# Performance work log

Measured on AMD Instinct MI355X. Metric: run time of the kernel, lower is better.

Reference implementation:

```python
import jax, jax.numpy as jnp
import numpy as np
from functools import partial

B, C, H, W = 256, 3, 128, 128

def _conv(x, w, b, pad):
    y = jax.lax.conv_general_dilated(x, w, (1, 1), [(pad, pad), (pad, pad)],
                                     dimension_numbers=('NCHW', 'OIHW', 'NCHW'))
    return y + b[None, :, None, None]

def _maxpool2(x):
    return jax.lax.reduce_window(x, -jnp.inf, jax.lax.max, (1, 1, 2, 2), (1, 1, 2, 2), 'VALID')

def _linear(x, w, b):
    return x @ w.T + b

def _handcrafted(images):
    # uint8 quantization: floor(x*255); inputs in [0,1) so no wraparound
    img8 = jnp.floor(images * 255.0)                      # [B,3,H,W]
    brightness = img8.mean(axis=(-2, -1))                 # [B,3]
    contrast = img8.std(axis=(-2, -1))                    # [B,3] (ddof=0, numpy default)
    # cv2.Sobel ksize=3, BORDER_REFLECT_101 == jnp.pad 'reflect'; cv2 does correlation
    kx = jnp.array([[-1., 0., 1.], [-2., 0., 2.], [-1., 0., 1.]], dtype=img8.dtype)
    ky = kx.T
    k = jnp.stack([kx, ky])[:, None]                      # [2,1,3,3]
    p = jnp.pad(img8, ((0, 0), (0, 0), (1, 1), (1, 1)), mode='reflect')
    s = jax.lax.conv_general_dilated(p.reshape(B * 3, 1, H + 2, W + 2), k, (1, 1),
                                     'VALID', dimension_numbers=('NCHW', 'OIHW', 'NCHW'))
    edge = jnp.sqrt(s[:, 0] ** 2 + s[:, 1] ** 2).mean(axis=(-2, -1)).reshape(B, 3)
    return jnp.concatenate([edge, brightness, contrast], axis=1)  # [B,9]

def setup_inputs() -> dict:
    key = jax.random.key(0)
    ks = jax.random.split(key, 20)
    g = lambda i, shape, fan: (jax.random.normal(ks[i], shape, jnp.float32) * (1.0 / np.sqrt(fan)))
    return {
        'images': jax.random.uniform(ks[0], (B, C, H, W), jnp.float32),
        'W1': g(1, (32, 3, 3, 3), 27), 'b1': jnp.zeros((32,), jnp.float32),
        'W2': g(2, (64, 32, 3, 3), 288), 'b2': jnp.zeros((64,), jnp.float32),
        'Wa': g(3, (1, 64, 7, 7), 64 * 49), 'ba': jnp.zeros((1,), jnp.float32),
        'Wfc': g(4, (50, 64 * 32 * 32), 64 * 32 * 32), 'bfc': jnp.zeros((50,), jnp.float32),
        'Wh1': g(5, (32, 9), 9), 'bh1': jnp.zeros((32,), jnp.float32),
        'Wh2': g(6, (64, 32), 32), 'bh2': jnp.zeros((64,), jnp.float32),
        'Wh3': g(7, (50, 64), 64), 'bh3': jnp.zeros((50,), jnp.float32),
        'Wf': g(8, (64, 100), 100), 'bf': jnp.zeros((64,), jnp.float32),
        'Wc': g(9, (1, 64), 64), 'bc': jnp.zeros((1,), jnp.float32),
    }

def reference(images, W1, b1, W2, b2, Wa, ba, Wfc, bfc,
              Wh1, bh1, Wh2, bh2, Wh3, bh3, Wf, bf, Wc, bc):
    # CNN branch
    x = jax.nn.relu(_conv(images, W1, b1, 1))
    x = _maxpool2(x)
    x = jax.nn.relu(_conv(x, W2, b2, 1))
    x = _maxpool2(x)                                      # [B,64,32,32]
    attn = jax.nn.sigmoid(_conv(x, Wa, ba, 3))            # spatial attention
    x = x * attn
    cnn_feat = jax.nn.relu(_linear(x.reshape(B, -1), Wfc, bfc))  # [B,50]
    # handcrafted branch
    f = _handcrafted(images)                              # [B,9]
    h = jax.nn.relu(_linear(f, Wh1, bh1))
    h = jax.nn.relu(_linear(h, Wh2, bh2))
    h = jax.nn.relu(_linear(h, Wh3, bh3))                 # [B,50]
    fused = jax.nn.relu(_linear(jnp.concatenate([cnn_feat, h], axis=1), Wf, bf))
    logits = _linear(fused, Wc, bc)
    return jax.nn.sigmoid(logits)
```

## Files before the change

kernel.cpp:

```cpp
#include <hip/hip_runtime.h>
#include <stdint.h>

typedef __bf16 bf16x8 __attribute__((ext_vector_type(8)));
typedef float f32x4 __attribute__((ext_vector_type(4)));

__device__ inline float bf2f(uint16_t u) {
    uint32_t x = ((uint32_t)u) << 16;
    float f;
    __builtin_memcpy(&f, &x, 4);
    return f;
}
__device__ inline uint16_t f2bf(float f) {
    uint32_t x;
    __builtin_memcpy(&x, &f, 4);
    uint32_t r = (x + 0x7FFFu + ((x >> 16) & 1u)) >> 16;
    return (uint16_t)r;
}

__global__ __launch_bounds__(256) void k_prep_small(const float* __restrict__ W2,
                                                    const float* __restrict__ W1,
                                                    const float* __restrict__ Wa,
                                                    uint16_t* __restrict__ wA,
                                                    uint16_t* __restrict__ wA1c,
                                                    uint16_t* __restrict__ waP) {
    int bid = blockIdx.x;
    int tid = threadIdx.x;
    if (bid < 72) {
        int j = bid * 256 + tid;
        if (j >= 18432) return;
        int t = j >> 11, rem = j & 2047, oc = rem >> 5, ic = rem & 31;
        int dy = t / 3, dx = t - dy * 3;
        wA[j] = f2bf(W2[(oc * 32 + ic) * 9 + dy * 3 + dx]);
    } else if (bid < 84) {
        int j = (bid - 72) * 256 + tid;
        if (j >= 3072) return;
        int dy = j >> 10, rem = j & 1023, oc = rem >> 5, k = rem & 31;
        int dx = k >> 2, ic = k & 3;
        uint16_t v = 0;
        if (dx < 3 && ic < 3) v = f2bf(W1[((oc * 3 + ic) * 3 + dy) * 3 + dx]);
        wA1c[j] = v;
    } else {
        int j = (bid - 84) * 256 + tid;
        if (j >= 4096) return;
        int chunk = j >> 10, ks = (j >> 9) & 1, tl = (j >> 5) & 15, ch = j & 31;
        int t = chunk * 16 + tl;
        int cg = ks * 32 + ch;
        waP[j] = (t < 49) ? f2bf(Wa[cg * 49 + t]) : (uint16_t)0;
    }
}

__global__ __launch_bounds__(256) void k_prep_wfc(const float* __restrict__ Wfc,
                                                  uint16_t* __restrict__ wfcb) {
    int o = blockIdx.x;
    int pb = blockIdx.y;
    int ch = threadIdx.x & 63;
    int pr = threadIdx.x >> 6;
    const float* src = Wfc + (size_t)o * 65536 + ch * 1024;
    uint16_t* dst = wfcb + (size_t)o * 65536 + ch;
#pragma unroll 4
    for (int i = 0; i < 16; ++i) {
        int px = pb * 64 + i * 4 + pr;
        dst[(size_t)px * 64] = f2bf(src[px]);
    }
}

__global__ __launch_bounds__(256) void k_handcrafted(const float* __restrict__ img,
                                                     float* __restrict__ f) {
    __shared__ float p[128 * 129];
    int c = blockIdx.x, b = blockIdx.y;
    const float* src = img + (((size_t)(b * 3 + c)) << 14);
    int tid = threadIdx.x;
    float sum = 0.f, sumsq = 0.f;
    for (int it = 0; it < 64; ++it) {
        int idx = tid + (it << 8);
        int r = idx >> 7, cc = idx & 127;
        float v = floorf(src[idx] * 255.0f);
        p[r * 129 + cc] = v;
        sum += v;
        sumsq += v * v;
    }
    __syncthreads();
    {
        int r = tid >> 1;
        int c0 = (tid & 1) * 64;
        int rm = (r == 0) ? 1 : (r - 1), rp = (r == 127) ? 126 : (r + 1);
        const float* Pm = &p[rm * 129];
        const float* P0 = &p[r * 129];
        const float* Pp = &p[rp * 129];
        float am, a0, ap, bm, b0, bp, cm, c0v, cp;
        if (c0 == 0) {
            a0 = Pm[0]; ap = Pm[1]; am = ap;
            b0 = P0[0]; bp = P0[1]; bm = bp;
            c0v = Pp[0]; cp = Pp[1]; cm = cp;
        } else {
            am = Pm[63]; a0 = Pm[64]; ap = Pm[65];
            bm = P0[63]; b0 = P0[64]; bp = P0[65];
            cm = Pp[63]; c0v = Pp[64]; cp = Pp[65];
        }
        float esum = 0.f;
        for (int i = 0; i < 64; ++i) {
            float gx = (ap - am) + 2.f * (bp - bm) + (cp - cm);
            float gy = (cm + 2.f * c0v + cp) - (am + 2.f * a0 + ap);
            esum += sqrtf(gx * gx + gy * gy);
            if (i < 63) {
                int nc = c0 + i + 2;
                am = a0; a0 = ap;
                bm = b0; b0 = bp;
                cm = c0v; c0v = cp;
                if (nc <= 127) {
                    ap = Pm[nc];
                    bp = P0[nc];
                    cp = Pp[nc];
                } else {
                    ap = am;
                    bp = bm;
                    cp = cm;
                }
            }
        }
        for (int off = 32; off; off >>= 1) {
            sum += __shfl_down(sum, off);
            sumsq += __shfl_down(sumsq, off);
            esum += __shfl_down(esum, off);
        }
        __syncthreads();
        int w = tid >> 6;
        if ((tid & 63) == 0) {
            p[w * 3 + 0] = sum;
            p[w * 3 + 1] = sumsq;
            p[w * 3 + 2] = esum;
        }
        __syncthreads();
        if (tid == 0) {
            float S = 0.f, Q = 0.f, E = 0.f;
            for (int i = 0; i < 4; ++i) {
                S += p[i * 3 + 0];
                Q += p[i * 3 + 1];
                E += p[i * 3 + 2];
            }
            const float inv = 1.0f / 16384.0f;
            float mean = S * inv;
            float var = Q * inv - mean * mean;
            f[b * 16 + c] = E * inv;
            f[b * 16 + 3 + c] = mean;
            f[b * 16 + 6 + c] = sqrtf(fmaxf(var, 0.f));
        }
    }
}

__global__ __launch_bounds__(256) void k_conv1_mfma(const float* __restrict__ img,
                                                    const uint16_t* __restrict__ wA1c,
                                                    const float* __restrict__ b1,
                                                    uint16_t* __restrict__ pooled1) {
    __shared__ uint16_t s_nhwc[18 * 34 * 4 + 32];
    __shared__ uint16_t s_out[8 * 16 * 32];
    const int tile = blockIdx.x;
    const int b = blockIdx.y;
    const int ty = tile >> 2, tx = tile & 3;
    const int Y0 = ty * 16, X0 = tx * 32;
    const int tid = threadIdx.x;

    for (int j = tid; j < 612; j += 256) {
        int r = j / 34, sc = j - r * 34;
        int gy = Y0 - 1 + r, gx = X0 - 1 + sc;
        uint16_t d[4] = {0, 0, 0, 0};
        if ((unsigned)gy < 128u && (unsigned)gx < 128u) {
            size_t base = (((size_t)b * 3) << 14) + (gy << 7) + gx;
#pragma unroll
            for (int ic = 0; ic < 3; ++ic) d[ic] = f2bf(img[base + ((size_t)ic << 14)]);
        }
        *(uint2*)&s_nhwc[j * 4] = *(uint2*)d;
    }

    const int wv = tid >> 6, lane = tid & 63;
    const int rowl = lane & 15, kg = lane >> 4;

    bf16x8 afr[3][2];
#pragma unroll
    for (int dy = 0; dy < 3; ++dy)
#pragma unroll
        for (int g = 0; g < 2; ++g)
            afr[dy][g] = *(const bf16x8*)(wA1c + dy * 1024 + (g * 16 + rowl) * 32 + kg * 8);
    float bias[2][4];
#pragma unroll
    for (int g = 0; g < 2; ++g)
#pragma unroll
        for (int r = 0; r < 4; ++r)
            bias[g][r] = b1[g * 16 + kg * 4 + r];

    __syncthreads();

#pragma unroll
    for (int pr = 0; pr < 2; ++pr) {
#pragma unroll
        for (int seg = 0; seg < 2; ++seg) {
            const int y0 = wv * 4 + pr * 2;
            const int xl = seg * 16 + rowl;
            bf16x8 bw[4];
#pragma unroll
            for (int rr = 0; rr < 4; ++rr) {
                const uint16_t* rp = &s_nhwc[((y0 + rr) * 34 + xl + kg * 2) * 4];
                uint2 lo = *(const uint2*)rp;
                uint2 hi = *(const uint2*)(rp + 4);
                union { uint2 u[2]; bf16x8 v; } u;
                u.u[0] = lo;
                u.u[1] = hi;
                bw[rr] = u.v;
            }
            f32x4 acc0[2], acc1[2];
#pragma unroll
            for (int g = 0; g < 2; ++g)
#pragma unroll
                for (int r = 0; r < 4; ++r) {
                    acc0[g][r] = bias[g][r];
                    acc1[g][r] = bias[g][r];
                }
#pragma unroll
            for (int dy = 0; dy < 3; ++dy)
#pragma unroll
                for (int g = 0; g < 2; ++g) {
                    acc0[g] = __builtin_amdgcn_mfma_f32_16x16x32_bf16(afr[dy][g], bw[dy], acc0[g], 0, 0, 0);
                    acc1[g] = __builtin_amdgcn_mfma_f32_16x16x32_bf16(afr[dy][g], bw[dy + 1], acc1[g], 0, 0, 0);
                }
#pragma unroll
            for (int g = 0; g < 2; ++g)
#pragma unroll
                for (int r = 0; r < 4; ++r) {
                    float m = fmaxf(acc0[g][r], acc1[g][r]);
                    m = fmaxf(m, 0.f);
                    float o = fmaxf(m, __shfl_xor(m, 1));
                    if (!(lane & 1)) {
                        int prow = wv * 2 + pr;
                        int pcol = seg * 8 + (rowl >> 1);
                        int oc = g * 16 + kg * 4 + r;
                        s_out[(prow * 16 + pcol) * 32 + oc] = f2bf(o);
                    }
                }
        }
    }
    __syncthreads();
    for (int u = tid; u < 512; u += 256) {
        int px = u >> 2, c = u & 3;
        int prow = px >> 4, pcol = px & 15;
        uint4 v = *(const uint4*)&s_out[px * 32 + c * 8];
        ((uint4*)pooled1)[((((size_t)b << 12) + (ty * 8 + prow) * 64 + tx * 16 + pcol) << 2) + c] = v;
    }
}

__global__ __launch_bounds__(256) void k_conv2_mfma(const uint16_t* __restrict__ pooled1,
                                                    const uint16_t* __restrict__ wA,
                                                    const float* __restrict__ b2v,
                                                    uint16_t* __restrict__ pooled2n) {
    __shared__ uint16_t s_in[10 * 34 * 32];
    __shared__ uint16_t s_out[64 * 64];
    const int bx = blockIdx.x;
    const int b = blockIdx.y;
    const int tx = bx >> 3, ty = bx & 7;
    const int X0 = tx * 32, Y0 = ty * 8;
    const int tid = threadIdx.x;

    for (int j = tid; j < 1360; j += 256) {
        int r = j / 136;
        int rem = j - r * 136;
        int px = rem >> 2, c4 = rem & 3;
        int gy = Y0 - 1 + r, gx = X0 - 1 + px;
        uint4 v = make_uint4(0, 0, 0, 0);
        if ((unsigned)gy < 64u && (unsigned)gx < 64u)
            v = ((const uint4*)pooled1)[((((size_t)b << 12) + gy * 64 + gx) << 2) + c4];
        *(uint4*)&s_in[(r * 34 + px) * 32 + c4 * 8] = v;
    }

    const int wv = tid >> 6, lane = tid & 63;
    const int ocq = wv & 1, xth = wv >> 1;
    const int rowl = lane & 15, kg = lane >> 4;

    bf16x8 afr[9][2];
#pragma unroll
    for (int t = 0; t < 9; ++t)
#pragma unroll
        for (int g = 0; g < 2; ++g) {
            afr[t][g] = *(const bf16x8*)(wA + t * 2048 + (ocq * 32 + g * 16 + rowl) * 32 + kg * 8);
            asm volatile("" : "+v"(afr[t][g]));
        }
    float bias[2][4];
#pragma unroll
    for (int g = 0; g < 2; ++g)
#pragma unroll
        for (int r = 0; r < 4; ++r)
            bias[g][r] = b2v[ocq * 32 + g * 16 + kg * 4 + r];

    __syncthreads();

#pragma unroll
    for (int h = 0; h < 2; ++h) {
        f32x4 acc[4][2];
#pragma unroll
        for (int y = 0; y < 4; ++y)
#pragma unroll
            for (int g = 0; g < 2; ++g)
#pragma unroll
                for (int r = 0; r < 4; ++r) acc[y][g][r] = bias[g][r];

#pragma unroll
        for (int rl = 0; rl < 6; ++rl) {
            const int r = 4 * h + rl;
            bf16x8 R[3];
#pragma unroll
            for (int dx = 0; dx < 3; ++dx) {
                int pix = r * 34 + xth * 16 + rowl + dx;
                R[dx] = *(const bf16x8*)(s_in + pix * 32 + kg * 8);
            }
#pragma unroll
            for (int dyp = 0; dyp < 3; ++dyp) {
                const int y = rl - dyp;
                if (y >= 0 && y < 4) {
#pragma unroll
                    for (int dx = 0; dx < 3; ++dx) {
                        const int t = dyp * 3 + dx;
#pragma unroll
                        for (int g = 0; g < 2; ++g)
                            acc[y][g] = __builtin_amdgcn_mfma_f32_16x16x32_bf16(afr[t][g], R[dx], acc[y][g], 0, 0, 0);
                    }
                }
            }
        }
#pragma unroll
        for (int i = 0; i < 2; ++i) {
#pragma unroll
            for (int g = 0; g < 2; ++g)
#pragma unroll
                for (int rr = 0; rr < 4; ++rr) {
                    float m = fmaxf(acc[2 * i][g][rr], acc[2 * i + 1][g][rr]);
                    m = fmaxf(m, 0.f);
                    float o = fmaxf(m, __shfl_xor(m, 1));
                    if (!(lane & 1)) {
                        int oc = ocq * 32 + g * 16 + kg * 4 + rr;
                        int pxl = xth * 8 + (rowl >> 1);
                        int pl = (h * 2 + i) * 16 + pxl;
                        s_out[pl * 64 + (oc ^ ((pxl & 7) << 3))] = f2bf(o);
                    }
                }
        }
    }
    __syncthreads();
    const int PY0 = ty * 4, PX0 = tx * 16;
    for (int u = tid; u < 512; u += 256) {
        int pl = u >> 3, c = u & 7;
        int py = pl >> 4, pxl = pl & 15;
        uint4 v = *(const uint4*)&s_out[pl * 64 + ((c ^ (pxl & 7)) << 3)];
        *(uint4*)&pooled2n[((((size_t)b << 10) + (PY0 + py) * 32 + PX0 + pxl) << 6) + c * 8] = v;
    }
}

__global__ __launch_bounds__(256) void k_attn_gemm(const uint16_t* __restrict__ pooled2n,
                                                   const uint16_t* __restrict__ waP,
                                                   const float* __restrict__ ba,
                                                   float* __restrict__ attn) {
    __shared__ uint16_t P[448 * 70];
    const int qt = blockIdx.x;
    const int b = blockIdx.y;
    const int tid = threadIdx.x;
    const int R0 = qt * 8;
    const int wv = tid >> 6, lane = tid & 63;
    const int rowl = lane & 15, kg = lane >> 4;

    bf16x8 afr[4][2];
#pragma unroll
    for (int c = 0; c < 4; ++c)
#pragma unroll
        for (int ks = 0; ks < 2; ++ks)
            afr[c][ks] = *(const bf16x8*)(waP + ((c * 2 + ks) * 16 + rowl) * 32 + kg * 8);

    for (int nt = wv; nt < 28; nt += 4) {
        int hpx = nt * 16 + rowl;
        int hrow = hpx >> 5, hcol = hpx & 31;
        int gy = R0 - 3 + hrow;
        bf16x8 bf0, bf1;
        if ((unsigned)gy < 32u) {
            const uint16_t* src = pooled2n + ((((size_t)b << 10) + (gy << 5) + hcol) << 6);
            bf0 = *(const bf16x8*)(src + kg * 8);
            bf1 = *(const bf16x8*)(src + 32 + kg * 8);
        } else {
            union { uint4 u; bf16x8 v; } z;
            z.u = make_uint4(0, 0, 0, 0);
            bf0 = z.v;
            bf1 = z.v;
        }
        f32x4 acc[4];
#pragma unroll
        for (int c = 0; c < 4; ++c)
#pragma unroll
            for (int r = 0; r < 4; ++r) acc[c][r] = 0.f;
#pragma unroll
        for (int c = 0; c < 4; ++c) {
            acc[c] = __builtin_amdgcn_mfma_f32_16x16x32_bf16(afr[c][0], bf0, acc[c], 0, 0, 0);
            acc[c] = __builtin_amdgcn_mfma_f32_16x16x32_bf16(afr[c][1], bf1, acc[c], 0, 0, 0);
        }
#pragma unroll
        for (int c = 0; c < 4; ++c) {
            uint32_t lo = (uint32_t)f2bf(acc[c][0]) | ((uint32_t)f2bf(acc[c][1]) << 16);
            uint32_t hi = (uint32_t)f2bf(acc[c][2]) | ((uint32_t)f2bf(acc[c][3]) << 16);
            uint16_t* dst = &P[hpx * 70 + c * 16 + kg * 4];
            *(uint32_t*)dst = lo;
            *(uint32_t*)(dst + 2) = hi;
        }
    }
    __syncthreads();

    const int pyl = tid >> 5, px = tid & 31;
    float v = ba[0];
#pragma unroll
    for (int dy = 0; dy < 7; ++dy) {
        int hl = pyl + dy;
#pragma unroll
        for (int dx = 0; dx < 7; ++dx) {
            int qx = px + dx - 3;
            if ((unsigned)qx < 32u) v += bf2f(P[(hl * 32 + qx) * 70 + dy * 7 + dx]);
        }
    }
    attn[((size_t)b << 10) + qt * 256 + tid] = 1.f / (1.f + __expf(-v));
}

__global__ __launch_bounds__(256) void k_fc_mfma(const uint16_t* __restrict__ pooled2n,
                                                 const float* __restrict__ attn,
                                                 const uint16_t* __restrict__ wfcb,
                                                 float* __restrict__ partial) {
    __shared__ uint16_t xh[128 * 128];
    const int it = blockIdx.x;
    const int kc = blockIdx.y;
    const int b0 = it * 16;
    const int K0 = kc * 1024;
    const int tid = threadIdx.x;

    for (int j = tid; j < 2048; j += 256) {
        int im = j >> 7, k8 = j & 127;
        int bimg = b0 + im;
        int gk = K0 + k8 * 8;
        int px = gk >> 6, ch0 = gk & 63;
        uint4 pv = *(const uint4*)&pooled2n[((((size_t)bimg << 10) + px) << 6) + ch0];
        float a = attn[((size_t)bimg << 10) + px];
        uint16_t s[8];
        *(uint4*)s = pv;
        uint16_t d[8];
#pragma unroll
        for (int i = 0; i < 8; ++i) d[i] = f2bf(bf2f(s[i]) * a);
        *(uint4*)&xh[k8 * 128 + im * 8] = *(uint4*)d;
    }

    const int wv = tid >> 6, lane = tid & 63;
    const int rowl = lane & 15, kg = lane >> 4;
    const uint16_t* wbase = wfcb + (size_t)(wv * 16 + rowl) * 65536 + K0 + kg * 8;

    __syncthreads();

    f32x4 acc = {0.f, 0.f, 0.f, 0.f};
#pragma unroll 4
    for (int kk = 0; kk < 32; ++kk) {
        bf16x8 af = *(const bf16x8*)(wbase + kk * 32);
        bf16x8 bf = *(const bf16x8*)&xh[(kk * 4 + kg) * 128 + rowl * 8];
        acc = __builtin_amdgcn_mfma_f32_16x16x32_bf16(af, bf, acc, 0, 0, 0);
    }
    float* pp = &partial[(((size_t)kc * 256 + (b0 + rowl)) << 6) + wv * 16 + kg * 4];
    *(f32x4*)pp = acc;
}

__global__ __launch_bounds__(64) void k_head(const float* __restrict__ fbuf,
                                             const float* __restrict__ partial,
                                             const float* __restrict__ Wh1, const float* __restrict__ bh1,
                                             const float* __restrict__ Wh2, const float* __restrict__ bh2,
                                             const float* __restrict__ Wh3, const float* __restrict__ bh3,
                                             const float* __restrict__ bfc,
                                             const float* __restrict__ Wf, const float* __restrict__ bf_,
                                             const float* __restrict__ Wc, const float* __restrict__ bc,
                                             float* __restrict__ out) {
    __shared__ float fl[9];
    __shared__ float h1[32];
    __shared__ float h2[64];
    __shared__ float cat[100];
    int b = blockIdx.x;
    int l = threadIdx.x;
    if (l < 9) fl[l] = fbuf[b * 16 + l];
    __syncthreads();
    if (l < 32) {
        float a = bh1[l];
        for (int i = 0; i < 9; ++i) a += fl[i] * Wh1[l * 9 + i];
        h1[l] = fmaxf(a, 0.f);
    }
    __syncthreads();
    {
        float a = bh2[l];
        for (int i = 0; i < 32; ++i) a += h1[i] * Wh2[l * 32 + i];
        h2[l] = fmaxf(a, 0.f);
    }
    __syncthreads();
    if (l < 50) {
        float a = bh3[l];
        for (int i = 0; i < 64; ++i) a += h2[i] * Wh3[l * 64 + i];
        cat[50 + l] = fmaxf(a, 0.f);
        float s = bfc[l];
        for (int kc2 = 0; kc2 < 64; ++kc2) s += partial[(((size_t)kc2 * 256 + b) << 6) + l];
        cat[l] = fmaxf(s, 0.f);
    }
    __syncthreads();
    float a = bf_[l];
    for (int i = 0; i < 100; ++i) a += cat[i] * Wf[l * 100 + i];
    a = fmaxf(a, 0.f);
    float v = a * Wc[l];
    for (int off = 32; off; off >>= 1) v += __shfl_down(v, off);
    if (l == 0) out[b] = 1.f / (1.f + __expf(-(v + bc[0])));
}

extern "C" void kernel_launch(void* const* d_in, const int* in_sizes, int n_in,
                              void* d_out, int out_size, void* d_ws, size_t ws_size,
                              hipStream_t stream) {
    const float* images = (const float*)d_in[0];
    const float* W1 = (const float*)d_in[1];
    const float* b1 = (const float*)d_in[2];
    const float* W2 = (const float*)d_in[3];
    const float* b2 = (const float*)d_in[4];
    const float* Wa = (const float*)d_in[5];
    const float* ba = (const float*)d_in[6];
    const float* Wfc = (const float*)d_in[7];
    const float* bfc = (const float*)d_in[8];
    const float* Wh1 = (const float*)d_in[9];
    const float* bh1 = (const float*)d_in[10];
    const float* Wh2 = (const float*)d_in[11];
    const float* bh2 = (const float*)d_in[12];
    const float* Wh3 = (const float*)d_in[13];
    const float* bh3 = (const float*)d_in[14];
    const float* Wf = (const float*)d_in[15];
    const float* bf_ = (const float*)d_in[16];
    const float* Wc = (const float*)d_in[17];
    const float* bc = (const float*)d_in[18];

    const size_t NEEDED = 102828032;
    if (ws_size < NEEDED) return;

    char* ws = (char*)d_ws;
    uint16_t* pooled1 = (uint16_t*)ws;
    uint16_t* pooled2n = (uint16_t*)(ws + 67108864);
    float* attn = (float*)(ws + 100663296);
    float* fbuf = (float*)(ws + 101711872);
    uint16_t* wA = (uint16_t*)(ws + 102776832);
    uint16_t* wA1c = (uint16_t*)(ws + 102813696);
    uint16_t* waP = (uint16_t*)(ws + 102819840);
    uint16_t* wfcb = (uint16_t*)ws;
    float* partial = (float*)(ws + 16777216);
    float* out = (float*)d_out;

    hipLaunchKernelGGL(k_prep_small, dim3(100), dim3(256), 0, stream, W2, W1, Wa, wA, wA1c, waP);
    hipLaunchKernelGGL(k_handcrafted, dim3(3, 256), dim3(256), 0, stream, images, fbuf);
    hipLaunchKernelGGL(k_conv1_mfma, dim3(32, 256), dim3(256), 0, stream, images, wA1c, b1, pooled1);
    hipLaunchKernelGGL(k_conv2_mfma, dim3(16, 256), dim3(256), 0, stream, pooled1, wA, b2, pooled2n);
    hipLaunchKernelGGL(k_prep_wfc, dim3(50, 16), dim3(256), 0, stream, Wfc, wfcb);
    hipLaunchKernelGGL(k_attn_gemm, dim3(4, 256), dim3(256), 0, stream, pooled2n, waP, ba, attn);
    hipLaunchKernelGGL(k_fc_mfma, dim3(16, 64), dim3(256), 0, stream, pooled2n, attn, wfcb, partial);
    hipLaunchKernelGGL(k_head, dim3(256), dim3(64), 0, stream, fbuf, partial,
                       Wh1, bh1, Wh2, bh2, Wh3, bh3, bfc, Wf, bf_, Wc, bc, out);
}
```

Before: 201.4 us.

## Transpose Wfc through shared memory, restructure conv2 row loop, remap fc grid

k_prep_wfc now loads Wfc rows with coalesced float4 reads, stages bf16 values in a padded shared tile, and writes the channel-major layout with ushort4 stores. This replaces the strided per-element scatter. k_conv2_mfma drops the rolling 6-row window over two halves in favour of a loop over 4 pooled row pairs, each loading 4 input rows. That lowers live accumulator registers, and the asm register pin on the A fragments is removed, at the cost of some repeated LDS reads. k_fc_mfma switches to a 1D grid with the K-chunk index varying fastest, which changes block scheduling order and L2 locality.

```diff
diff --git a/kernel.cpp b/kernel.cpp
--- a/kernel.cpp
+++ b/kernel.cpp
@@ -51,16 +51,33 @@
 
 __global__ __launch_bounds__(256) void k_prep_wfc(const float* __restrict__ Wfc,
                                                   uint16_t* __restrict__ wfcb) {
+    __shared__ uint16_t sT[64][132];
     int o = blockIdx.x;
-    int pb = blockIdx.y;
-    int ch = threadIdx.x & 63;
-    int pr = threadIdx.x >> 6;
-    const float* src = Wfc + (size_t)o * 65536 + ch * 1024;
-    uint16_t* dst = wfcb + (size_t)o * 65536 + ch;
-#pragma unroll 4
-    for (int i = 0; i < 16; ++i) {
-        int px = pb * 64 + i * 4 + pr;
-        dst[(size_t)px * 64] = f2bf(src[px]);
+    int px0 = blockIdx.y * 128;
+    int tid = threadIdx.x;
+#pragma unroll
+    for (int p = 0; p < 8; ++p) {
+        int idx = p * 256 + tid;
+        int ch = idx >> 5, c4 = idx & 31;
+        float4 v = *(const float4*)&Wfc[(size_t)o * 65536 + ch * 1024 + px0 + c4 * 4];
+        ushort4 u;
+        u.x = f2bf(v.x);
+        u.y = f2bf(v.y);
+        u.z = f2bf(v.z);
+        u.w = f2bf(v.w);
+        *(ushort4*)&sT[ch][c4 * 4] = u;
+    }
+    __syncthreads();
+#pragma unroll
+    for (int p = 0; p < 8; ++p) {
+        int idx = p * 256 + tid;
+        int pxl = idx >> 4, c = idx & 15;
+        ushort4 u;
+        u.x = sT[4 * c + 0][pxl];
+        u.y = sT[4 * c + 1][pxl];
+        u.z = sT[4 * c + 2][pxl];
+        u.w = sT[4 * c + 3][pxl];
+        *(ushort4*)&wfcb[(size_t)o * 65536 + (size_t)(px0 + pxl) * 64 + c * 4] = u;
     }
 }
 
@@ -278,10 +295,8 @@
 #pragma unroll
     for (int t = 0; t < 9; ++t)
 #pragma unroll
-        for (int g = 0; g < 2; ++g) {
+        for (int g = 0; g < 2; ++g)
             afr[t][g] = *(const bf16x8*)(wA + t * 2048 + (ocq * 32 + g * 16 + rowl) * 32 + kg * 8);
-            asm volatile("" : "+v"(afr[t][g]));
-        }
     float bias[2][4];
 #pragma unroll
     for (int g = 0; g < 2; ++g)
@@ -291,56 +306,48 @@
 
     __syncthreads();
 
-#pragma unroll
-    for (int h = 0; h < 2; ++h) {
-        f32x4 acc[4][2];
-#pragma unroll
-        for (int y = 0; y < 4; ++y)
+    for (int yp = 0; yp < 4; ++yp) {
+        f32x4 acc[2][2];
+#pragma unroll
+        for (int p = 0; p < 2; ++p)
 #pragma unroll
             for (int g = 0; g < 2; ++g)
 #pragma unroll
-                for (int r = 0; r < 4; ++r) acc[y][g][r] = bias[g][r];
-
-#pragma unroll
-        for (int rl = 0; rl < 6; ++rl) {
-            const int r = 4 * h + rl;
-            bf16x8 R[3];
+                for (int r = 0; r < 4; ++r) acc[p][g][r] = bias[g][r];
+
+        bf16x8 bfr[4][3];
+#pragma unroll
+        for (int rr = 0; rr < 4; ++rr)
 #pragma unroll
             for (int dx = 0; dx < 3; ++dx) {
-                int pix = r * 34 + xth * 16 + rowl + dx;
-                R[dx] = *(const bf16x8*)(s_in + pix * 32 + kg * 8);
+                int pix = (2 * yp + rr) * 34 + xth * 16 + rowl + dx;
+                bfr[rr][dx] = *(const bf16x8*)(s_in + pix * 32 + kg * 8);
             }
 #pragma unroll
-            for (int dyp = 0; dyp < 3; ++dyp) {
-                const int y = rl - dyp;
-                if (y >= 0 && y < 4) {
-#pragma unroll
-                    for (int dx = 0; dx < 3; ++dx) {
-                        const int t = dyp * 3 + dx;
-#pragma unroll
-                        for (int g = 0; g < 2; ++g)
-                            acc[y][g] = __builtin_amdgcn_mfma_f32_16x16x32_bf16(afr[t][g], R[dx], acc[y][g], 0, 0, 0);
-                    }
+        for (int dy = 0; dy < 3; ++dy)
+#pragma unroll
+            for (int dx = 0; dx < 3; ++dx) {
+                int t = dy * 3 + dx;
+#pragma unroll
+                for (int g = 0; g < 2; ++g) {
+                    acc[0][g] = __builtin_amdgcn_mfma_f32_16x16x32_bf16(afr[t][g], bfr[dy][dx], acc[0][g], 0, 0, 0);
+                    acc[1][g] = __builtin_amdgcn_mfma_f32_16x16x32_bf16(afr[t][g], bfr[dy + 1][dx], acc[1][g], 0, 0, 0);
                 }
             }
-        }
-#pragma unroll
-        for (int i = 0; i < 2; ++i) {
-#pragma unroll
-            for (int g = 0; g < 2; ++g)
-#pragma unroll
-                for (int rr = 0; rr < 4; ++rr) {
-                    float m = fmaxf(acc[2 * i][g][rr], acc[2 * i + 1][g][rr]);
-                    m = fmaxf(m, 0.f);
-                    float o = fmaxf(m, __shfl_xor(m, 1));
-                    if (!(lane & 1)) {
-                        int oc = ocq * 32 + g * 16 + kg * 4 + rr;
-                        int pxl = xth * 8 + (rowl >> 1);
-                        int pl = (h * 2 + i) * 16 + pxl;
-                        s_out[pl * 64 + (oc ^ ((pxl & 7) << 3))] = f2bf(o);
-                    }
+#pragma unroll
+        for (int g = 0; g < 2; ++g)
+#pragma unroll
+            for (int r = 0; r < 4; ++r) {
+                float m = fmaxf(acc[0][g][r], acc[1][g][r]);
+                m = fmaxf(m, 0.f);
+                float o = fmaxf(m, __shfl_xor(m, 1));
+                if (!(lane & 1)) {
+                    int oc = ocq * 32 + g * 16 + kg * 4 + r;
+                    int pxl = xth * 8 + (rowl >> 1);
+                    int pl = yp * 16 + pxl;
+                    s_out[pl * 64 + (oc ^ ((pxl & 7) << 3))] = f2bf(o);
                 }
-        }
+            }
     }
     __syncthreads();
     const int PY0 = ty * 4, PX0 = tx * 16;
@@ -426,8 +433,9 @@
                                                  const uint16_t* __restrict__ wfcb,
                                                  float* __restrict__ partial) {
     __shared__ uint16_t xh[128 * 128];
-    const int it = blockIdx.x;
-    const int kc = blockIdx.y;
+    const int wg = blockIdx.x;
+    const int it = wg >> 6;
+    const int kc = wg & 63;
     const int b0 = it * 16;
     const int K0 = kc * 1024;
     const int tid = threadIdx.x;
@@ -552,9 +560,9 @@
     hipLaunchKernelGGL(k_handcrafted, dim3(3, 256), dim3(256), 0, stream, images, fbuf);
     hipLaunchKernelGGL(k_conv1_mfma, dim3(32, 256), dim3(256), 0, stream, images, wA1c, b1, pooled1);
     hipLaunchKernelGGL(k_conv2_mfma, dim3(16, 256), dim3(256), 0, stream, pooled1, wA, b2, pooled2n);
-    hipLaunchKernelGGL(k_prep_wfc, dim3(50, 16), dim3(256), 0, stream, Wfc, wfcb);
+    hipLaunchKernelGGL(k_prep_wfc, dim3(50, 8), dim3(256), 0, stream, Wfc, wfcb);
     hipLaunchKernelGGL(k_attn_gemm, dim3(4, 256), dim3(256), 0, stream, pooled2n, waP, ba, attn);
-    hipLaunchKernelGGL(k_fc_mfma, dim3(16, 64), dim3(256), 0, stream, pooled2n, attn, wfcb, partial);
+    hipLaunchKernelGGL(k_fc_mfma, dim3(1024), dim3(256), 0, stream, pooled2n, attn, wfcb, partial);
     hipLaunchKernelGGL(k_head, dim3(256), dim3(64), 0, stream, fbuf, partial,
                        Wh1, bh1, Wh2, bh2, Wh3, bh3, bfc, Wf, bf_, Wc, bc, out);
 }
```

Result: faster. 171.0 us (-15.1%).
